# Optimization experiments

Measured on AMD Instinct MI355X. Metric: run time of the kernel, lower is better.

The kernel has to match this reference:

```python
import jax, jax.numpy as jnp
import numpy as np

# ---- column/activation layout (matches transformer_info init kwarg) ----
N_COLS = 20          # continuous data columns
MODES = 50           # VGM modes per column (gumbel-softmax width)
SPAN = MODES + 1     # 1 tanh scalar + MODES gumbel logits
IN_DIM = 2048
OUT_DIM = N_COLS * SPAN  # 1020
TAU = 0.2
B = 16384
EPS = 1e-9

_spans = []
for i in range(N_COLS):
    st = i * SPAN
    _spans.append((st, st + 1, 0))          # tanh span (alpha)
    _spans.append((st + 1, st + SPAN, 1))   # gumbel-softmax span (beta/d)
N_SEG = len(_spans)

_seg = np.zeros(OUT_DIM, np.int32)   # segment id per output feature
_typ = np.zeros(OUT_DIM, np.int32)   # 0 = tanh, 1 = gumbel-softmax
for si, (s, e, t) in enumerate(_spans):
    _seg[s:e] = si
    _typ[s:e] = t
SEG = jnp.asarray(_seg)
TYP = jnp.asarray(_typ)


def setup_inputs() -> dict:
    key = jax.random.key(0)
    kx, kw, kb, ku = jax.random.split(key, 4)
    bound = 1.0 / np.sqrt(IN_DIM)  # init_bounded(dim=input_dim)
    x = jax.random.normal(kx, (B, IN_DIM), dtype=jnp.float32)
    W = jax.random.uniform(kw, (IN_DIM, OUT_DIM), minval=-bound, maxval=bound, dtype=jnp.float32)
    b = jax.random.uniform(kb, (OUT_DIM,), minval=-bound, maxval=bound, dtype=jnp.float32)
    u = jax.random.uniform(ku, (B, OUT_DIM), dtype=jnp.float32)  # uniform driving gumbel noise
    return {"x": x, "W": W, "b": b, "u": u}


def _segment_softmax(z):
    # softmax over each transformer_info span, fused via segment ops.
    zT = z.T  # [D, B]
    m = jax.ops.segment_max(zT, SEG, num_segments=N_SEG)      # [S, B]
    e = jnp.exp(zT - m[SEG])
    s = jax.ops.segment_sum(e, SEG, num_segments=N_SEG)       # [S, B]
    return (e / s[SEG]).T  # [B, D]


def reference(x, W, b, u):
    outputs = x @ W + b  # [B, OUT_DIM]
    # Gumbel(0,1) noise from uniform u
    g = -jnp.log(-jnp.log(jnp.clip(u, EPS, 1.0 - EPS)))
    soft = _segment_softmax((outputs + g) / TAU)
    # type 0 -> tanh, type 1 -> gumbel-softmax (single fused select)
    data_t = jnp.where(TYP == 0, jnp.tanh(outputs), soft)
    return outputs, data_t
```

## Files before the change

### kernel.cpp

```cpp
#include <hip/hip_runtime.h>
#include <stdint.h>

#define MDIM 16384
#define NDIM 1020
#define KDIM 2048
#define NPAD 1024
#define TK   (KDIM / 64)

typedef __attribute__((ext_vector_type(4))) float f32x4;
typedef __attribute__((ext_vector_type(8))) short short8;

#define MFMA16(a, b, c) __builtin_amdgcn_mfma_f32_16x16x32_bf16((a), (b), (c), 0, 0, 0)

template <int OFF>
static __device__ __forceinline__ short8 dsr(unsigned addr) {
    short8 r;
    asm volatile("ds_read_b128 %0, %1 offset:%2" : "=v"(r) : "v"(addr), "i"(OFF));
    return r;
}

__device__ __forceinline__ unsigned short f2bf(float f) {
    unsigned int u = __float_as_uint(f);
    unsigned int r = (u + 0x7FFFu + ((u >> 16) & 1u)) >> 16;
    return (unsigned short)r;
}

__global__ void prep_w_kernel(const float* __restrict__ W,
                              unsigned short* __restrict__ Wt) {
    const int id = blockIdx.x * 256 + threadIdx.x;
    const int n0 = (id & 255) * 4;
    const int k0 = (id >> 8) * 4;
    float a[4][4];
    if (n0 < NDIM) {
#pragma unroll
        for (int i = 0; i < 4; ++i) {
            const float* p = W + (size_t)(k0 + i) * NDIM + n0;
            a[i][0] = p[0]; a[i][1] = p[1]; a[i][2] = p[2]; a[i][3] = p[3];
        }
    } else {
#pragma unroll
        for (int i = 0; i < 4; ++i)
#pragma unroll
            for (int j = 0; j < 4; ++j) a[i][j] = 0.f;
    }
#pragma unroll
    for (int j = 0; j < 4; ++j) {
        uint2 p;
        p.x = (unsigned)f2bf(a[0][j]) | ((unsigned)f2bf(a[1][j]) << 16);
        p.y = (unsigned)f2bf(a[2][j]) | ((unsigned)f2bf(a[3][j]) << 16);
        *(uint2*)(Wt + (size_t)(n0 + j) * KDIM + k0) = p;
    }
}

__global__ void prep_x_kernel(const float* __restrict__ x,
                              unsigned short* __restrict__ Xb) {
    const size_t total = (size_t)MDIM * KDIM;
    const size_t stride = (size_t)gridDim.x * 256 * 8;
    for (size_t i = ((size_t)blockIdx.x * 256 + threadIdx.x) * 8; i < total; i += stride) {
        const float4 v0 = *(const float4*)(x + i);
        const float4 v1 = *(const float4*)(x + i + 4);
        uint4 p;
        p.x = (unsigned)f2bf(v0.x) | ((unsigned)f2bf(v0.y) << 16);
        p.y = (unsigned)f2bf(v0.z) | ((unsigned)f2bf(v0.w) << 16);
        p.z = (unsigned)f2bf(v1.x) | ((unsigned)f2bf(v1.y) << 16);
        p.w = (unsigned)f2bf(v1.z) | ((unsigned)f2bf(v1.w) << 16);
        *(uint4*)(Xb + i) = p;
    }
}

extern "C" __global__ __launch_bounds__(512, 2) void gemm8_kernel(
    const unsigned short* __restrict__ Xb,
    const unsigned short* __restrict__ Wt,
    const float* __restrict__ bias,
    float* __restrict__ out) {
    extern __shared__ unsigned short lds_raw[];

    const int tid  = threadIdx.x;
    const int lane = tid & 63;
    const int wid  = tid >> 6;
    const int wr   = wid >> 2;
    const int wc   = wid & 3;

    const int bid = blockIdx.x;
    const int swz = (bid & 7) * 32 + (bid >> 3);
    const int bm  = swz >> 2;
    const int bn  = swz & 3;

    const int srow = wid * 8 + (lane >> 3);
    const int scb  = ((lane & 7) ^ (lane >> 3)) * 8;
    const unsigned short* aS = Xb + (size_t)(bm * 256 + srow) * KDIM + scb;
    const unsigned short* bS = Wt + (size_t)(bn * 256 + srow) * KDIM + scb;

#define STAGE(BUFI, OP, STRIPE, S) do {                                          \
    const size_t ks_ = (size_t)(((S) * 64) & (KDIM - 1));                        \
    const unsigned short* sp_ =                                                  \
        ((OP) ? bS : aS) + (size_t)((STRIPE) * 64) * KDIM + ks_;                 \
    __builtin_amdgcn_global_load_lds(                                            \
        (const __attribute__((address_space(1))) unsigned int*)sp_,              \
        (__attribute__((address_space(3))) unsigned int*)(lds_raw +              \
            (BUFI) * 32768 + (OP) * 16384 + ((STRIPE) * 64 + wid * 8) * 64),     \
        16, 0, 0);                                                               \
} while (0)

#define VMCNT4 do {                                                              \
    asm volatile("s_waitcnt vmcnt(4)" ::: "memory");                             \
    __builtin_amdgcn_sched_barrier(0);                                           \
} while (0)

    const unsigned ldsbase =
        (unsigned)(uintptr_t)(__attribute__((address_space(3))) unsigned short*)lds_raw;
    const unsigned l15 = lane & 15, hi = lane >> 4, l7 = lane & 7;
    const unsigned c0 = (unsigned)((0 * 4 + hi) ^ l7) << 4;
    const unsigned c1 = (unsigned)((1 * 4 + hi) ^ l7) << 4;
    const unsigned pbA = ldsbase + (unsigned)(wr * 128 + l15) * 128;
    const unsigned pbB = ldsbase + 32768u + (unsigned)(wc * 64 + l15) * 128;

    f32x4 acc[8][4];
#pragma unroll
    for (int i = 0; i < 8; ++i)
#pragma unroll
        for (int j = 0; j < 4; ++j) {
            f32x4 z = {0.f, 0.f, 0.f, 0.f};
            acc[i][j] = z;
        }

    STAGE(0, 0, 0, 0); STAGE(0, 0, 1, 0); STAGE(0, 0, 2, 0); STAGE(0, 0, 3, 0);
    STAGE(0, 1, 0, 0); STAGE(0, 1, 1, 0); STAGE(0, 1, 2, 0); STAGE(0, 1, 3, 0);
    STAGE(1, 1, 0, 1); STAGE(1, 1, 1, 1); STAGE(1, 1, 2, 1); STAGE(1, 1, 3, 1);
    STAGE(1, 0, 0, 1); STAGE(1, 0, 2, 1);
    VMCNT4;
    __builtin_amdgcn_s_barrier();

#define PH_TAIL                                                       \
    __builtin_amdgcn_s_barrier();                                     \
    asm volatile("s_waitcnt lgkmcnt(0)" ::: "memory");                \
    __builtin_amdgcn_sched_barrier(0);                                \
    __builtin_amdgcn_s_setprio(1);

#define PH_MFMA(MF0)                                                  \
    _Pragma("unroll")                                                 \
    for (int nf = 0; nf < 4; ++nf) {                                  \
        acc[MF0][nf]     = MFMA16(af0[0], bfv[nf][0], acc[MF0][nf]);      \
        acc[MF0][nf]     = MFMA16(af0[1], bfv[nf][1], acc[MF0][nf]);      \
        acc[MF0 + 1][nf] = MFMA16(af1[0], bfv[nf][0], acc[MF0 + 1][nf]);  \
        acc[MF0 + 1][nf] = MFMA16(af1[1], bfv[nf][1], acc[MF0 + 1][nf]);  \
    }                                                                 \
    __builtin_amdgcn_sched_barrier(0);                                \
    __builtin_amdgcn_s_setprio(0);

#define RDA(MF0)                                                      \
    af0[0] = dsr<(MF0) * 2048>(aadr0);                                \
    af0[1] = dsr<(MF0) * 2048>(aadr1);                                \
    af1[0] = dsr<(MF0) * 2048 + 2048>(aadr0);                         \
    af1[1] = dsr<(MF0) * 2048 + 2048>(aadr1);

#define RDB(NF)                                                       \
    bfv[NF][0] = dsr<(NF) * 2048>(badr0);                             \
    bfv[NF][1] = dsr<(NF) * 2048>(badr1);

    for (int t = 0; t < TK; ++t) {
        const int buf = t & 1;
        const int nb  = buf ^ 1;
        const unsigned bo = (unsigned)buf << 16;
        const unsigned aadr0 = pbA + bo + c0, aadr1 = pbA + bo + c1;
        const unsigned badr0 = pbB + bo + c0, badr1 = pbB + bo + c1;
        short8 bfv[4][2];
        short8 af0[2], af1[2];

        RDB(0) RDB(1) RDB(2) RDB(3)
        RDA(0)
        STAGE(nb, 0, 1, t + 1);
        STAGE(nb, 0, 3, t + 1);
        PH_TAIL
        PH_MFMA(0)
        __builtin_amdgcn_s_barrier();

        RDA(2)
        STAGE(buf, 1, 0, t + 2);
        STAGE(buf, 1, 1, t + 2);
        PH_TAIL
        PH_MFMA(2)
        __builtin_amdgcn_s_barrier();

        RDA(4)
        STAGE(buf, 1, 2, t + 2);
        STAGE(buf, 1, 3, t + 2);
        PH_TAIL
        PH_MFMA(4)
        __builtin_amdgcn_s_barrier();

        RDA(6)
        STAGE(buf, 0, 0, t + 2);
        STAGE(buf, 0, 2, t + 2);
        PH_TAIL
        PH_MFMA(6)
        VMCNT4;
        __builtin_amdgcn_s_barrier();
    }

#pragma unroll
    for (int nf = 0; nf < 4; ++nf) {
        const int col = bn * 256 + wc * 64 + nf * 16 + (lane & 15);
        if (col < NDIM) {
            const float bv = bias[col];
#pragma unroll
            for (int mf = 0; mf < 8; ++mf) {
                const int row = bm * 256 + wr * 128 + mf * 16 + ((lane >> 4) << 2);
                float* op = out + (size_t)row * NDIM + col;
#pragma unroll
                for (int r = 0; r < 4; ++r)
                    op[(size_t)r * NDIM] = acc[mf][nf][r] + bv;
            }
        }
    }
#undef STAGE
#undef VMCNT4
#undef PH_TAIL
#undef PH_MFMA
#undef RDA
#undef RDB
}

__global__ void gemm_bf_kernel(const unsigned short* __restrict__ Xb,
                               const unsigned short* __restrict__ Wt,
                               const float* __restrict__ bias,
                               float* __restrict__ out) {
    __shared__ __align__(16) unsigned short As[128][32];
    __shared__ __align__(16) unsigned short Bs[128][32];

    const int tid  = threadIdx.x;
    const int lane = tid & 63;
    const int wid  = tid >> 6;
    const int wr   = wid >> 1;
    const int wc   = wid & 1;
    const int bn   = blockIdx.x;
    const int bm   = blockIdx.y;

    f32x4 acc[4][4];
#pragma unroll
    for (int i = 0; i < 4; ++i)
#pragma unroll
        for (int j = 0; j < 4; ++j) {
            f32x4 z = {0.f, 0.f, 0.f, 0.f};
            acc[i][j] = z;
        }

    const unsigned short* abase =
        Xb + (size_t)(bm * 128 + wid * 16 + (lane >> 2)) * KDIM + (lane & 3) * 8;
    const unsigned short* bbase =
        Wt + (size_t)(bn * 128 + wid * 16 + (lane >> 2)) * KDIM + (lane & 3) * 8;

    for (int kt = 0; kt < KDIM; kt += 32) {
#pragma unroll
        for (int j = 0; j < 2; ++j)
            __builtin_amdgcn_global_load_lds(
                (const __attribute__((address_space(1))) unsigned int*)(abase + (size_t)j * 64 * KDIM + kt),
                (__attribute__((address_space(3))) unsigned int*)(&As[j * 64 + wid * 16][0]),
                16, 0, 0);
#pragma unroll
        for (int j = 0; j < 2; ++j)
            __builtin_amdgcn_global_load_lds(
                (const __attribute__((address_space(1))) unsigned int*)(bbase + (size_t)j * 64 * KDIM + kt),
                (__attribute__((address_space(3))) unsigned int*)(&Bs[j * 64 + wid * 16][0]),
                16, 0, 0);
        __syncthreads();

        short8 af[4], bfr[4];
#pragma unroll
        for (int mi = 0; mi < 4; ++mi)
            af[mi] = *(const short8*)&As[wr * 64 + mi * 16 + (lane & 15)][(lane >> 4) * 8];
#pragma unroll
        for (int ni = 0; ni < 4; ++ni)
            bfr[ni] = *(const short8*)&Bs[wc * 64 + ni * 16 + (lane & 15)][(lane >> 4) * 8];

#pragma unroll
        for (int mi = 0; mi < 4; ++mi)
#pragma unroll
            for (int ni = 0; ni < 4; ++ni)
                acc[mi][ni] = MFMA16(af[mi], bfr[ni], acc[mi][ni]);

        __syncthreads();
    }

#pragma unroll
    for (int ni = 0; ni < 4; ++ni) {
        const int col = bn * 128 + wc * 64 + ni * 16 + (lane & 15);
        if (col < NDIM) {
            const float bv = bias[col];
#pragma unroll
            for (int mi = 0; mi < 4; ++mi) {
                const int row = bm * 128 + wr * 64 + mi * 16 + ((lane >> 4) << 2);
                float* op = out + (size_t)row * NDIM + col;
#pragma unroll
                for (int r = 0; r < 4; ++r)
                    op[(size_t)r * NDIM] = acc[mi][ni][r] + bv;
            }
        }
    }
}

__global__ void act_kernel(const float* __restrict__ outp,
                           const float* __restrict__ u,
                           float* __restrict__ dt) {
    const int lane  = threadIdx.x & 63;
    const int gwave = (blockIdx.x * 256 + threadIdx.x) >> 6;
    const int nwave = gridDim.x * 4;
    const int total = MDIM * 20;
    const float NEG_INF = -__builtin_inff();

    for (int unit = gwave; unit < total; unit += nwave) {
        const int row = unit / 20;
        const int sp  = unit - row * 20;
        const size_t base = (size_t)row * NDIM + sp * 51;

        float o = 0.f, uu = 0.5f;
        if (lane < 51) {
            o  = outp[base + lane];
            uu = u[base + lane];
        }
        const bool soft = (lane >= 1) && (lane < 51);

        const float uc = fmaxf(uu, 1e-9f);
        const float g  = -__logf(-__logf(uc));
        float z = soft ? (o + g) * 5.0f : NEG_INF;

        float m = z;
#pragma unroll
        for (int off = 32; off; off >>= 1) m = fmaxf(m, __shfl_xor(m, off));
        float e = soft ? __expf(z - m) : 0.f;
        float s = e;
#pragma unroll
        for (int off = 32; off; off >>= 1) s += __shfl_xor(s, off);

        float res;
        if (lane == 0) {
            const float ex = __expf(-2.0f * fabsf(o));
            const float t  = (1.0f - ex) / (1.0f + ex);
            res = copysignf(t, o);
        } else {
            res = e / s;
        }
        if (lane < 51) dt[base + lane] = res;
    }
}

extern "C" void kernel_launch(void* const* d_in, const int* in_sizes, int n_in,
                              void* d_out, int out_size, void* d_ws, size_t ws_size,
                              hipStream_t stream) {
    const float* x = (const float*)d_in[0];
    const float* W = (const float*)d_in[1];
    const float* b = (const float*)d_in[2];
    const float* u = (const float*)d_in[3];
    float* out = (float*)d_out;
    float* dt  = out + (size_t)MDIM * NDIM;
    unsigned short* Wt = (unsigned short*)d_ws;
    unsigned short* Xb = Wt + (size_t)NPAD * KDIM;

    prep_w_kernel<<<512, 256, 0, stream>>>(W, Wt);
    prep_x_kernel<<<2048, 256, 0, stream>>>(x, Xb);

    const hipError_t attr_ok = hipFuncSetAttribute(
        (const void*)gemm8_kernel, hipFuncAttributeMaxDynamicSharedMemorySize, 131072);
    if (attr_ok == hipSuccess) {
        gemm8_kernel<<<256, 512, 131072, stream>>>(Xb, Wt, b, out);
    } else {
        gemm_bf_kernel<<<dim3(8, 128), 256, 0, stream>>>(Xb, Wt, b, out);
    }

    act_kernel<<<8192, 256, 0, stream>>>(out, u, dt);
}
```

Before: 191.8 us.

## Restructure GEMM main loop into two phases with B-fragment register double buffering

Reorganizes the 256x256 bf16 MFMA main loop from four phases per K-tile into two larger phases of 32 MFMAs each. B fragments for the next tile are prefetched from LDS into a second register set (ping-pong bfvP/bfvQ) while the current tile computes, and the loop is unrolled by two to alternate buffers. The global-load wait threshold moves from vmcnt(4) to vmcnt(2) to match the new issue order. The aim is fewer barriers and better overlap of LDS reads with MFMA work, at the cost of more VGPRs, which can lower occupancy or cause spills. The ordering of LDS prefetch reads against buffer overwrites is also tricky to get right.

```diff
diff --git a/kernel.cpp b/kernel.cpp
--- a/kernel.cpp
+++ b/kernel.cpp
@@ -99,13 +99,63 @@
         (const __attribute__((address_space(1))) unsigned int*)sp_,              \
         (__attribute__((address_space(3))) unsigned int*)(lds_raw +              \
             (BUFI) * 32768 + (OP) * 16384 + ((STRIPE) * 64 + wid * 8) * 64),     \
-        16, 0, 0);                                                               \
+        16, 0, 0);                                                              \
 } while (0)
 
-#define VMCNT4 do {                                                              \
-    asm volatile("s_waitcnt vmcnt(4)" ::: "memory");                             \
-    __builtin_amdgcn_sched_barrier(0);                                           \
+#define VMCNT2 do {                                                             \
+    asm volatile("s_waitcnt vmcnt(2)" ::: "memory");                            \
+    __builtin_amdgcn_sched_barrier(0);                                          \
 } while (0)
+
+#define PH_TAIL                                                       \
+    __builtin_amdgcn_s_barrier();                                     \
+    asm volatile("s_waitcnt lgkmcnt(0)" ::: "memory");                \
+    __builtin_amdgcn_sched_barrier(0);                                \
+    __builtin_amdgcn_s_setprio(1);
+
+#define PH_END                                                        \
+    __builtin_amdgcn_sched_barrier(0);                                \
+    __builtin_amdgcn_s_setprio(0);
+
+#define MFMA32(MB, CUR)                                                         \
+    _Pragma("unroll")                                                           \
+    for (int k2 = 0; k2 < 2; ++k2)                                              \
+        _Pragma("unroll")                                                       \
+        for (int mi = 0; mi < 4; ++mi)                                          \
+            _Pragma("unroll")                                                   \
+            for (int nf = 0; nf < 4; ++nf)                                      \
+                acc[(MB) + mi][nf] =                                            \
+                    MFMA16(af[mi][k2], CUR[nf][k2], acc[(MB) + mi][nf]);
+
+#define TILE(T, BUF, NB, CUR, NXT)                                              \
+  {                                                      \
+    af[0][0]=dsr<0*2048>(aA##BUF##_0); af[0][1]=dsr<0*2048>(aA##BUF##_1);       \
+    af[1][0]=dsr<1*2048>(aA##BUF##_0); af[1][1]=dsr<1*2048>(aA##BUF##_1);       \
+    af[2][0]=dsr<2*2048>(aA##BUF##_0); af[2][1]=dsr<2*2048>(aA##BUF##_1);       \
+    af[3][0]=dsr<3*2048>(aA##BUF##_0); af[3][1]=dsr<3*2048>(aA##BUF##_1);       \
+    NXT[0][0]=dsr<0*2048>(bB##NB##_0); NXT[0][1]=dsr<0*2048>(bB##NB##_1);       \
+    NXT[1][0]=dsr<1*2048>(bB##NB##_0); NXT[1][1]=dsr<1*2048>(bB##NB##_1);       \
+    STAGE(NB, 0, 1, (T) + 1); STAGE(NB, 0, 3, (T) + 1);                         \
+    STAGE(BUF, 1, 0, (T) + 2); STAGE(BUF, 1, 1, (T) + 2);                       \
+    PH_TAIL                                                                     \
+    MFMA32(0, CUR)                                                              \
+    PH_END                                                                      \
+    __builtin_amdgcn_s_barrier();                                               \
+                                                         \
+    af[0][0]=dsr<4*2048>(aA##BUF##_0); af[0][1]=dsr<4*2048>(aA##BUF##_1);       \
+    af[1][0]=dsr<5*2048>(aA##BUF##_0); af[1][1]=dsr<5*2048>(aA##BUF##_1);       \
+    af[2][0]=dsr<6*2048>(aA##BUF##_0); af[2][1]=dsr<6*2048>(aA##BUF##_1);       \
+    af[3][0]=dsr<7*2048>(aA##BUF##_0); af[3][1]=dsr<7*2048>(aA##BUF##_1);       \
+    NXT[2][0]=dsr<2*2048>(bB##NB##_0); NXT[2][1]=dsr<2*2048>(bB##NB##_1);       \
+    NXT[3][0]=dsr<3*2048>(bB##NB##_0); NXT[3][1]=dsr<3*2048>(bB##NB##_1);       \
+    STAGE(BUF, 1, 2, (T) + 2); STAGE(BUF, 1, 3, (T) + 2);                       \
+    STAGE(BUF, 0, 0, (T) + 2); STAGE(BUF, 0, 2, (T) + 2);                       \
+    PH_TAIL                                                                     \
+    MFMA32(4, CUR)                                                              \
+    PH_END                                                                      \
+    VMCNT2;                                                                     \
+    __builtin_amdgcn_s_barrier();                                               \
+  }
 
     const unsigned ldsbase =
         (unsigned)(uintptr_t)(__attribute__((address_space(3))) unsigned short*)lds_raw;
@@ -114,6 +164,10 @@
     const unsigned c1 = (unsigned)((1 * 4 + hi) ^ l7) << 4;
     const unsigned pbA = ldsbase + (unsigned)(wr * 128 + l15) * 128;
     const unsigned pbB = ldsbase + 32768u + (unsigned)(wc * 64 + l15) * 128;
+    const unsigned aA0_0 = pbA + c0,          aA0_1 = pbA + c1;
+    const unsigned aA1_0 = pbA + 65536u + c0, aA1_1 = pbA + 65536u + c1;
+    const unsigned bB0_0 = pbB + c0,          bB0_1 = pbB + c1;
+    const unsigned bB1_0 = pbB + 65536u + c0, bB1_1 = pbB + 65536u + c1;
 
     f32x4 acc[8][4];
 #pragma unroll
@@ -123,79 +177,28 @@
             f32x4 z = {0.f, 0.f, 0.f, 0.f};
             acc[i][j] = z;
         }
+
+    short8 af[4][2];
+    short8 bfvP[4][2], bfvQ[4][2];
 
     STAGE(0, 0, 0, 0); STAGE(0, 0, 1, 0); STAGE(0, 0, 2, 0); STAGE(0, 0, 3, 0);
     STAGE(0, 1, 0, 0); STAGE(0, 1, 1, 0); STAGE(0, 1, 2, 0); STAGE(0, 1, 3, 0);
     STAGE(1, 1, 0, 1); STAGE(1, 1, 1, 1); STAGE(1, 1, 2, 1); STAGE(1, 1, 3, 1);
     STAGE(1, 0, 0, 1); STAGE(1, 0, 2, 1);
-    VMCNT4;
+    VMCNT2;
     __builtin_amdgcn_s_barrier();
 
-#define PH_TAIL                                                       \
-    __builtin_amdgcn_s_barrier();                                     \
-    asm volatile("s_waitcnt lgkmcnt(0)" ::: "memory");                \
-    __builtin_amdgcn_sched_barrier(0);                                \
-    __builtin_amdgcn_s_setprio(1);
-
-#define PH_MFMA(MF0)                                                  \
-    _Pragma("unroll")                                                 \
-    for (int nf = 0; nf < 4; ++nf) {                                  \
-        acc[MF0][nf]     = MFMA16(af0[0], bfv[nf][0], acc[MF0][nf]);      \
-        acc[MF0][nf]     = MFMA16(af0[1], bfv[nf][1], acc[MF0][nf]);      \
-        acc[MF0 + 1][nf] = MFMA16(af1[0], bfv[nf][0], acc[MF0 + 1][nf]);  \
-        acc[MF0 + 1][nf] = MFMA16(af1[1], bfv[nf][1], acc[MF0 + 1][nf]);  \
-    }                                                                 \
-    __builtin_amdgcn_sched_barrier(0);                                \
-    __builtin_amdgcn_s_setprio(0);
-
-#define RDA(MF0)                                                      \
-    af0[0] = dsr<(MF0) * 2048>(aadr0);                                \
-    af0[1] = dsr<(MF0) * 2048>(aadr1);                                \
-    af1[0] = dsr<(MF0) * 2048 + 2048>(aadr0);                         \
-    af1[1] = dsr<(MF0) * 2048 + 2048>(aadr1);
-
-#define RDB(NF)                                                       \
-    bfv[NF][0] = dsr<(NF) * 2048>(badr0);                             \
-    bfv[NF][1] = dsr<(NF) * 2048>(badr1);
-
-    for (int t = 0; t < TK; ++t) {
-        const int buf = t & 1;
-        const int nb  = buf ^ 1;
-        const unsigned bo = (unsigned)buf << 16;
-        const unsigned aadr0 = pbA + bo + c0, aadr1 = pbA + bo + c1;
-        const unsigned badr0 = pbB + bo + c0, badr1 = pbB + bo + c1;
-        short8 bfv[4][2];
-        short8 af0[2], af1[2];
-
-        RDB(0) RDB(1) RDB(2) RDB(3)
-        RDA(0)
-        STAGE(nb, 0, 1, t + 1);
-        STAGE(nb, 0, 3, t + 1);
-        PH_TAIL
-        PH_MFMA(0)
-        __builtin_amdgcn_s_barrier();
-
-        RDA(2)
-        STAGE(buf, 1, 0, t + 2);
-        STAGE(buf, 1, 1, t + 2);
-        PH_TAIL
-        PH_MFMA(2)
-        __builtin_amdgcn_s_barrier();
-
-        RDA(4)
-        STAGE(buf, 1, 2, t + 2);
-        STAGE(buf, 1, 3, t + 2);
-        PH_TAIL
-        PH_MFMA(4)
-        __builtin_amdgcn_s_barrier();
-
-        RDA(6)
-        STAGE(buf, 0, 0, t + 2);
-        STAGE(buf, 0, 2, t + 2);
-        PH_TAIL
-        PH_MFMA(6)
-        VMCNT4;
-        __builtin_amdgcn_s_barrier();
+    bfvP[0][0]=dsr<0*2048>(bB0_0); bfvP[0][1]=dsr<0*2048>(bB0_1);
+    bfvP[1][0]=dsr<1*2048>(bB0_0); bfvP[1][1]=dsr<1*2048>(bB0_1);
+    bfvP[2][0]=dsr<2*2048>(bB0_0); bfvP[2][1]=dsr<2*2048>(bB0_1);
+    bfvP[3][0]=dsr<3*2048>(bB0_0); bfvP[3][1]=dsr<3*2048>(bB0_1);
+    asm volatile("s_waitcnt lgkmcnt(0)" ::: "memory");
+    __builtin_amdgcn_sched_barrier(0);
+    __builtin_amdgcn_s_barrier();
+
+    for (int t2 = 0; t2 < TK; t2 += 2) {
+        TILE(t2,     0, 1, bfvP, bfvQ)
+        TILE(t2 + 1, 1, 0, bfvQ, bfvP)
     }
 
 #pragma unroll
@@ -214,11 +217,11 @@
         }
     }
 #undef STAGE
-#undef VMCNT4
+#undef VMCNT2
 #undef PH_TAIL
-#undef PH_MFMA
-#undef RDA
-#undef RDB
+#undef PH_END
+#undef MFMA32
+#undef TILE
 }
 
 __global__ void gemm_bf_kernel(const unsigned short* __restrict__ Xb,
```

Result: slower. 205.5 us (+7.1%).
